# Optimization experiments

Measured on AMD Instinct MI355X. Metric: run time of the kernel, lower is better.

## Reference

```python
import jax, jax.numpy as jnp
import numpy as np

D_MODEL = 1024
NUM_HEADS = 16
D_K = D_MODEL // NUM_HEADS


def setup_inputs() -> dict:
    key = jax.random.key(0)
    ks = jax.random.split(key, 9)
    s = 1.0 / np.sqrt(D_MODEL)
    x = jax.random.normal(ks[0], (4, 2048, D_MODEL), dtype=jnp.float32)
    Wq = jax.random.uniform(ks[1], (D_MODEL, D_MODEL), jnp.float32, -s, s)
    bq = jax.random.uniform(ks[2], (D_MODEL,), jnp.float32, -s, s)
    Wk = jax.random.uniform(ks[3], (D_MODEL, D_MODEL), jnp.float32, -s, s)
    bk = jax.random.uniform(ks[4], (D_MODEL,), jnp.float32, -s, s)
    Wv = jax.random.uniform(ks[5], (D_MODEL, D_MODEL), jnp.float32, -s, s)
    bv = jax.random.uniform(ks[6], (D_MODEL,), jnp.float32, -s, s)
    Wo = jax.random.uniform(ks[7], (D_MODEL, D_MODEL), jnp.float32, -s, s)
    bo = jax.random.uniform(ks[8], (D_MODEL,), jnp.float32, -s, s)
    return {"x": x, "Wq": Wq, "bq": bq, "Wk": Wk, "bk": bk,
            "Wv": Wv, "bv": bv, "Wo": Wo, "bo": bo}


def reference(x, Wq, bq, Wk, bk, Wv, bv, Wo, bo):
    B, T, C = x.shape
    H, Dk = NUM_HEADS, D_K
    # linear projections (torch Linear: x @ W.T + b; here W stored as [in,out])
    q = (x @ Wq + bq).reshape(B, T, H, Dk).transpose(0, 2, 1, 3)  # [B,H,T,Dk]
    k = (x @ Wk + bk).reshape(B, T, H, Dk).transpose(0, 2, 1, 3)
    v = (x @ Wv + bv).reshape(B, T, H, Dk).transpose(0, 2, 1, 3)
    scores = jnp.einsum("bhtd,bhsd->bhts", q, k) / jnp.sqrt(jnp.float32(Dk))
    attn = jax.nn.softmax(scores, axis=-1)  # [B,H,T,T]
    context = jnp.einsum("bhts,bhsd->bhtd", attn, v)
    context = context.transpose(0, 2, 1, 3).reshape(B, T, C)
    return context @ Wo + bo
```

## Files before the change

kernel.cpp:

```cpp
#include <hip/hip_runtime.h>
#include <hip/hip_bf16.h>
#include <stdint.h>

typedef short bf16x8 __attribute__((ext_vector_type(8)));
typedef short bf16x4 __attribute__((ext_vector_type(4)));
typedef float f32x4  __attribute__((ext_vector_type(4)));

#define MFMA16(a, b, c) __builtin_amdgcn_mfma_f32_16x16x32_bf16((a), (b), (c), 0, 0, 0)

__device__ __forceinline__ unsigned short f2bf(float f) {
    union { float f; unsigned int u; } v; v.f = f;
    unsigned int u = v.u;
    u += 0x7fffu + ((u >> 16) & 1u);
    return (unsigned short)(u >> 16);
}

__device__ __forceinline__ unsigned int trunc_pk(float a, float b) {
    return (__float_as_uint(a) >> 16) | (__float_as_uint(b) & 0xffff0000u);
}

__device__ __forceinline__ float exp2f_fast(float x) {
#if __has_builtin(__builtin_amdgcn_exp2f)
    return __builtin_amdgcn_exp2f(x);
#else
    return exp2f(x);
#endif
}

__device__ __forceinline__ void g2lds16(const void* g, void* l) {
    __builtin_amdgcn_global_load_lds(
        (const __attribute__((address_space(1))) void*)g,
        (__attribute__((address_space(3))) void*)l, 16, 0, 0);
}


__global__ __launch_bounds__(256) void convert_x_kernel(
    const float4* __restrict__ src, ushort4* __restrict__ dst)
{
    int i = blockIdx.x * 256 + threadIdx.x;
    float4 v = src[i];
    ushort4 o;
    o.x = f2bf(v.x); o.y = f2bf(v.y); o.z = f2bf(v.z); o.w = f2bf(v.w);
    dst[i] = o;
}

__global__ __launch_bounds__(256) void transpose_w4_kernel(
    const float* __restrict__ W0, const float* __restrict__ W1,
    const float* __restrict__ W2, const float* __restrict__ W3,
    unsigned short* __restrict__ dst_base)
{
    __shared__ float tile[64][65];
    const int z = blockIdx.z;
    const float* src = (z == 0) ? W0 : (z == 1) ? W1 : (z == 2) ? W2 : W3;
    unsigned short* dst = dst_base + ((size_t)z << 20);
    const int k0 = blockIdx.x * 64, n0 = blockIdx.y * 64;
    const int tx = threadIdx.x & 63, ty = threadIdx.x >> 6;
    #pragma unroll
    for (int i = 0; i < 64; i += 4)
        tile[ty + i][tx] = src[(size_t)(k0 + ty + i) * 1024 + n0 + tx];
    __syncthreads();
    #pragma unroll
    for (int i = 0; i < 64; i += 4)
        dst[(size_t)(n0 + ty + i) * 1024 + k0 + tx] = f2bf(tile[tx][ty + i]);
}


#define QSCALE 0.18033688011112042f

template <int MODE>
__global__ __launch_bounds__(512, 2) void gemm256(
    const unsigned short* __restrict__ A, const unsigned short* __restrict__ Bt,
    const float* __restrict__ b0, const float* __restrict__ b1, const float* __restrict__ b2,
    unsigned short* __restrict__ Qb, unsigned short* __restrict__ Kb,
    unsigned short* __restrict__ Vt, float* __restrict__ out)
{
    __shared__ alignas(16) unsigned short As[2][256 * 64];
    __shared__ alignas(16) unsigned short Bs[2][128 * 64];

    const int t = threadIdx.x;
    const int m0 = blockIdx.y * 256, n0 = blockIdx.x * 128;
    const int lane = t & 63, w = t >> 6, quad = lane >> 4, c16 = lane & 15;
    const int moff = (w >> 1) * 64;
    const int noff = (w & 1) * 64;

    f32x4 acc[4][4];
    #pragma unroll
    for (int i = 0; i < 4; ++i)
        #pragma unroll
        for (int j = 0; j < 4; ++j)
            acc[i][j] = (f32x4){0.f, 0.f, 0.f, 0.f};

    const int sg = (t & 7) ^ ((t >> 3) & 7);
    const unsigned short* Agl = A  + (size_t)(m0 + (t >> 3)) * 1024 + sg * 8;
    const unsigned short* Bgl = Bt + (size_t)(n0 + (t >> 3)) * 1024 + sg * 8;
    unsigned short* Asl = &As[0][0] + t * 8;
    unsigned short* Bsl = &Bs[0][0] + t * 8;

    #pragma unroll
    for (int q = 0; q < 4; ++q)
        g2lds16(Agl + (size_t)q * 65536, Asl + q * 4096);
    #pragma unroll
    for (int q = 0; q < 2; ++q)
        g2lds16(Bgl + (size_t)q * 65536, Bsl + q * 4096);
    asm volatile("s_waitcnt vmcnt(0)" ::: "memory");
    __builtin_amdgcn_sched_barrier(0);
    __builtin_amdgcn_s_barrier();
    __builtin_amdgcn_sched_barrier(0);

    const int swz = c16 & 7;

    for (int kt = 0; kt < 16; ++kt) {
        const int buf = kt & 1;
        const unsigned short* Ab = &As[buf][0];
        const unsigned short* Bb = &Bs[buf][0];
        unsigned short* An = Asl + (buf ^ 1) * 16384;
        unsigned short* Bn = Bsl + (buf ^ 1) * 8192;
        const size_t knext = (size_t)(kt + 1) * 64;

        #pragma unroll
        for (int kh = 0; kh < 2; ++kh) {
            const int fgr = ((kh * 4 + quad) ^ swz) << 3;
            bf16x8 af[4], bfr[4];
            #pragma unroll
            for (int ms = 0; ms < 4; ++ms)
                af[ms] = *(const bf16x8*)(Ab + (moff + ms * 16 + c16) * 64 + fgr);
            #pragma unroll
            for (int ns = 0; ns < 4; ++ns)
                bfr[ns] = *(const bf16x8*)(Bb + (noff + ns * 16 + c16) * 64 + fgr);

            if (kt < 15) {
                if (kh == 0) {
                    g2lds16(Agl + knext,                      An);
                    g2lds16(Agl + knext + 65536,              An + 4096);
                    g2lds16(Bgl + knext,                      Bn);
                } else {
                    g2lds16(Agl + knext + 2 * 65536,          An + 2 * 4096);
                    g2lds16(Agl + knext + 3 * 65536,          An + 3 * 4096);
                    g2lds16(Bgl + knext + 65536,              Bn + 4096);
                }
            }

            __builtin_amdgcn_sched_barrier(0);
            __builtin_amdgcn_s_barrier();
            asm volatile("s_waitcnt lgkmcnt(0)" ::: "memory");
            __builtin_amdgcn_sched_barrier(0);

            __builtin_amdgcn_s_setprio(1);
            #pragma unroll
            for (int ms = 0; ms < 4; ++ms)
                #pragma unroll
                for (int ns = 0; ns < 4; ++ns)
                    acc[ms][ns] = MFMA16(af[ms], bfr[ns], acc[ms][ns]);
            __builtin_amdgcn_s_setprio(0);

            if (kh == 1) {
                asm volatile("s_waitcnt vmcnt(0)" ::: "memory");
            }
            __builtin_amdgcn_sched_barrier(0);
            __builtin_amdgcn_s_barrier();
            __builtin_amdgcn_sched_barrier(0);
        }
    }

    #pragma unroll
    for (int ns = 0; ns < 4; ++ns) {
        const int n = n0 + noff + ns * 16 + c16;
        if (MODE == 0) {
            const int mat = n >> 10, nn = n & 1023;
            const int h = nn >> 6, d = nn & 63;
            const float bias = (mat == 0) ? b0[nn] : ((mat == 1) ? b1[nn] : b2[nn]);
            #pragma unroll
            for (int ms = 0; ms < 4; ++ms) {
                const int mbase = m0 + moff + ms * 16 + quad * 4;
                const int b = mbase >> 11, tbase = mbase & 2047;
                const int bh = b * 16 + h;
                if (mat == 2) {
                    ushort4 pk;
                    pk.x = f2bf(acc[ms][ns][0] + bias);
                    pk.y = f2bf(acc[ms][ns][1] + bias);
                    pk.z = f2bf(acc[ms][ns][2] + bias);
                    pk.w = f2bf(acc[ms][ns][3] + bias);
                    *(ushort4*)(Vt + ((size_t)bh * 64 + d) * 2048 + tbase) = pk;
                } else {
                    #pragma unroll
                    for (int r = 0; r < 4; ++r) {
                        float v = acc[ms][ns][r] + bias;
                        if (mat == 0) v *= QSCALE;
                        unsigned short* dst = (mat == 0) ? Qb : Kb;
                        dst[((size_t)bh * 2048 + tbase + r) * 64 + d] = f2bf(v);
                    }
                }
            }
        } else {
            const float bias = b0[n];
            #pragma unroll
            for (int ms = 0; ms < 4; ++ms) {
                #pragma unroll
                for (int r = 0; r < 4; ++r) {
                    const int m = m0 + moff + ms * 16 + quad * 4 + r;
                    out[(size_t)m * 1024 + n] = acc[ms][ns][r] + bias;
                }
            }
        }
    }
}


__global__ __launch_bounds__(256, 4) void attn_kernel(
    const unsigned short* __restrict__ Qb, const unsigned short* __restrict__ Kb,
    const unsigned short* __restrict__ Vt, unsigned short* __restrict__ ctx)
{
    __shared__ alignas(16) unsigned short Ks[2][64 * 64];
    __shared__ alignas(16) unsigned short Vs[2][64 * 64];

    const int t = threadIdx.x, w = t >> 6, lane = t & 63;
    const int quad = lane >> 4, c16 = lane & 15;
    const int L = blockIdx.y * 16 + blockIdx.x;
    const int bh = ((L & 7) << 3) + (L >> 7);
    const int qt = (L >> 3) & 15;
    const int qbase = qt * 128 + w * 32;

    bf16x8 qf[2][2];
    #pragma unroll
    for (int mt = 0; mt < 2; ++mt) {
        const unsigned short* Qp = Qb + ((size_t)bh * 2048 + qbase + mt * 16 + c16) * 64;
        qf[mt][0] = *(const bf16x8*)(Qp + quad * 8);
        qf[mt][1] = *(const bf16x8*)(Qp + 32 + quad * 8);
    }

    float l_r[2] = {0.f, 0.f};
    f32x4 O[2][4];
    #pragma unroll
    for (int mt = 0; mt < 2; ++mt)
        #pragma unroll
        for (int dc = 0; dc < 4; ++dc) O[mt][dc] = (f32x4){0.f, 0.f, 0.f, 0.f};

    const int sgrp = (t & 7) ^ ((t >> 3) & 7);
    const unsigned short* Kgl = Kb + (size_t)bh * 131072 + (size_t)(t >> 3) * 64 + sgrp * 8;
    const unsigned short* Vgl = Vt + (size_t)bh * 131072 + (size_t)(t >> 3) * 2048 + sgrp * 8;
    const int tOff = t * 8;
    const f32x4 fzero = {0.f, 0.f, 0.f, 0.f};

    #pragma unroll
    for (int q = 0; q < 2; ++q) {
        g2lds16(Kgl + q * 2048,  Ks[0] + tOff + q * 2048);
        g2lds16(Vgl + (size_t)q * 65536, Vs[0] + tOff + q * 2048);
    }

    for (int it = 0; it < 32; ++it) {
        const int cur = it & 1;
        const unsigned short* Kc = Ks[cur];
        const unsigned short* Vc = Vs[cur];

        if (it < 31) {
            const int s0 = (it + 1) * 64;
            unsigned short* Kn = Ks[cur ^ 1] + tOff;
            unsigned short* Vn = Vs[cur ^ 1] + tOff;
            #pragma unroll
            for (int q = 0; q < 2; ++q) {
                g2lds16(Kgl + (size_t)s0 * 64 + q * 2048,    Kn + q * 2048);
                g2lds16(Vgl + s0 + (size_t)q * 65536,        Vn + q * 2048);
            }
            asm volatile("s_waitcnt vmcnt(4)" ::: "memory");
        } else {
            asm volatile("s_waitcnt vmcnt(0)" ::: "memory");
        }
        __builtin_amdgcn_sched_barrier(0);
        __builtin_amdgcn_s_barrier();
        __builtin_amdgcn_sched_barrier(0);

        #pragma unroll
        for (int ctp = 0; ctp < 2; ++ctp) {
            union { bf16x8 v; unsigned int d[4]; } af8[2];
            union { bf16x8 v; uint2 u[2]; } v8[4];

            #pragma unroll
            for (int ct2 = 0; ct2 < 2; ++ct2) {
                const int ct = ctp * 2 + ct2;
                const int key = ct * 16 + c16;
                const bf16x8 kf0 = *(const bf16x8*)(Kc + key * 64 + ((quad ^ (key & 7)) << 3));
                const bf16x8 kf1 = *(const bf16x8*)(Kc + key * 64 + (((4 + quad) ^ (key & 7)) << 3));

                const int g = ct * 2 + (quad >> 1);
                #pragma unroll
                for (int dc = 0; dc < 4; ++dc) {
                    const int d = dc * 16 + c16;
                    v8[dc].u[ct2] = *(const uint2*)(Vc + d * 64 + ((g ^ (d & 7)) << 3) + (quad & 1) * 4);
                }

                #pragma unroll
                for (int mt = 0; mt < 2; ++mt) {
                    f32x4 sa = MFMA16(kf0, qf[mt][0], fzero);
                    sa = MFMA16(kf1, qf[mt][1], sa);
                    const float p0 = exp2f_fast(sa[0]);
                    const float p1 = exp2f_fast(sa[1]);
                    const float p2 = exp2f_fast(sa[2]);
                    const float p3 = exp2f_fast(sa[3]);
                    l_r[mt] += (p0 + p1) + (p2 + p3);
                    af8[mt].d[ct2 * 2 + 0] = trunc_pk(p0, p1);
                    af8[mt].d[ct2 * 2 + 1] = trunc_pk(p2, p3);
                }
            }

            #pragma unroll
            for (int mt = 0; mt < 2; ++mt)
                #pragma unroll
                for (int dc = 0; dc < 4; ++dc)
                    O[mt][dc] = MFMA16(af8[mt].v, v8[dc].v, O[mt][dc]);
        }

        if (it < 31) {
            asm volatile("s_waitcnt lgkmcnt(0)" ::: "memory");
            __builtin_amdgcn_sched_barrier(0);
            __builtin_amdgcn_s_barrier();
            __builtin_amdgcn_sched_barrier(0);
        }
    }

    #pragma unroll
    for (int mt = 0; mt < 2; ++mt) {
        l_r[mt] += __shfl_xor(l_r[mt], 16);
        l_r[mt] += __shfl_xor(l_r[mt], 32);
    }

    const int b = bh >> 4, h = bh & 15;
    #pragma unroll
    for (int mt = 0; mt < 2; ++mt) {
        float inv[4];
        #pragma unroll
        for (int r = 0; r < 4; ++r)
            inv[r] = 1.0f / __shfl(l_r[mt], quad * 4 + r);
        #pragma unroll
        for (int dc = 0; dc < 4; ++dc)
            #pragma unroll
            for (int r = 0; r < 4; ++r) {
                const int row = qbase + mt * 16 + quad * 4 + r;
                ctx[((size_t)(b * 2048 + row)) * 1024 + h * 64 + dc * 16 + c16] =
                    f2bf(O[mt][dc][r] * inv[r]);
            }
    }
}


extern "C" void kernel_launch(void* const* d_in, const int* in_sizes, int n_in,
                              void* d_out, int out_size, void* d_ws, size_t ws_size,
                              hipStream_t stream)
{
    const float* x  = (const float*)d_in[0];
    const float* Wq = (const float*)d_in[1];
    const float* bq = (const float*)d_in[2];
    const float* Wk = (const float*)d_in[3];
    const float* bk = (const float*)d_in[4];
    const float* Wv = (const float*)d_in[5];
    const float* bv = (const float*)d_in[6];
    const float* Wo = (const float*)d_in[7];
    const float* bo = (const float*)d_in[8];
    float* out = (float*)d_out;

    char* ws = (char*)d_ws;
    unsigned short* xb    = (unsigned short*)(ws);
    unsigned short* Wqkvt = (unsigned short*)(ws + (16u << 20));
    unsigned short* Vt    = (unsigned short*)(ws + (24u << 20));
    unsigned short* Wot   = Wqkvt + (3u << 20);
    unsigned short* Qb    = (unsigned short*)((char*)d_out);
    unsigned short* Kb    = (unsigned short*)((char*)d_out + (16u << 20));

    convert_x_kernel<<<8192, 256, 0, stream>>>((const float4*)x, (ushort4*)xb);
    transpose_w4_kernel<<<dim3(16, 16, 4), 256, 0, stream>>>(Wq, Wk, Wv, Wo, Wqkvt);

    gemm256<0><<<dim3(24, 32), 512, 0, stream>>>(xb, Wqkvt, bq, bk, bv, Qb, Kb, Vt, nullptr);
    attn_kernel<<<dim3(16, 64), 256, 0, stream>>>(Qb, Kb, Vt, xb );
    gemm256<1><<<dim3(8, 32), 512, 0, stream>>>(xb, Wot, bo, nullptr, nullptr,
                                                nullptr, nullptr, nullptr, out);
}
```

Baseline: 277.0 us.

## Triple-buffer GEMM LDS prefetch and merge prep kernels into one launch

```diff
diff --git a/kernel.cpp b/kernel.cpp
--- a/kernel.cpp
+++ b/kernel.cpp
@@ -34,34 +34,35 @@
 }
 
 
-__global__ __launch_bounds__(256) void convert_x_kernel(
-    const float4* __restrict__ src, ushort4* __restrict__ dst)
-{
-    int i = blockIdx.x * 256 + threadIdx.x;
-    float4 v = src[i];
-    ushort4 o;
-    o.x = f2bf(v.x); o.y = f2bf(v.y); o.z = f2bf(v.z); o.w = f2bf(v.w);
-    dst[i] = o;
-}
-
-__global__ __launch_bounds__(256) void transpose_w4_kernel(
+__global__ __launch_bounds__(256) void prep_kernel(
+    const float4* __restrict__ src, ushort4* __restrict__ dst,
     const float* __restrict__ W0, const float* __restrict__ W1,
     const float* __restrict__ W2, const float* __restrict__ W3,
-    unsigned short* __restrict__ dst_base)
+    unsigned short* __restrict__ wdst_base)
 {
     __shared__ float tile[64][65];
-    const int z = blockIdx.z;
-    const float* src = (z == 0) ? W0 : (z == 1) ? W1 : (z == 2) ? W2 : W3;
-    unsigned short* dst = dst_base + ((size_t)z << 20);
-    const int k0 = blockIdx.x * 64, n0 = blockIdx.y * 64;
-    const int tx = threadIdx.x & 63, ty = threadIdx.x >> 6;
-    #pragma unroll
-    for (int i = 0; i < 64; i += 4)
-        tile[ty + i][tx] = src[(size_t)(k0 + ty + i) * 1024 + n0 + tx];
-    __syncthreads();
-    #pragma unroll
-    for (int i = 0; i < 64; i += 4)
-        dst[(size_t)(n0 + ty + i) * 1024 + k0 + tx] = f2bf(tile[tx][ty + i]);
+    const int id = blockIdx.x;
+    if (id < 8192) {
+        int i = id * 256 + threadIdx.x;
+        float4 v = src[i];
+        ushort4 o;
+        o.x = f2bf(v.x); o.y = f2bf(v.y); o.z = f2bf(v.z); o.w = f2bf(v.w);
+        dst[i] = o;
+    } else {
+        const int r = id - 8192;
+        const int z = r >> 8, rem = r & 255;
+        const float* wsrc = (z == 0) ? W0 : (z == 1) ? W1 : (z == 2) ? W2 : W3;
+        unsigned short* wdst = wdst_base + ((size_t)z << 20);
+        const int k0 = (rem & 15) * 64, n0 = (rem >> 4) * 64;
+        const int tx = threadIdx.x & 63, ty = threadIdx.x >> 6;
+        #pragma unroll
+        for (int i = 0; i < 64; i += 4)
+            tile[ty + i][tx] = wsrc[(size_t)(k0 + ty + i) * 1024 + n0 + tx];
+        __syncthreads();
+        #pragma unroll
+        for (int i = 0; i < 64; i += 4)
+            wdst[(size_t)(n0 + ty + i) * 1024 + k0 + tx] = f2bf(tile[tx][ty + i]);
+    }
 }
 
 
@@ -74,8 +75,8 @@
     unsigned short* __restrict__ Qb, unsigned short* __restrict__ Kb,
     unsigned short* __restrict__ Vt, float* __restrict__ out)
 {
-    __shared__ alignas(16) unsigned short As[2][256 * 64];
-    __shared__ alignas(16) unsigned short Bs[2][128 * 64];
+    __shared__ alignas(16) unsigned short As[3][256 * 64];
+    __shared__ alignas(16) unsigned short Bs[3][128 * 64];
 
     const int t = threadIdx.x;
     const int m0 = blockIdx.y * 256, n0 = blockIdx.x * 128;
@@ -93,29 +94,37 @@
     const int sg = (t & 7) ^ ((t >> 3) & 7);
     const unsigned short* Agl = A  + (size_t)(m0 + (t >> 3)) * 1024 + sg * 8;
     const unsigned short* Bgl = Bt + (size_t)(n0 + (t >> 3)) * 1024 + sg * 8;
-    unsigned short* Asl = &As[0][0] + t * 8;
-    unsigned short* Bsl = &Bs[0][0] + t * 8;
-
-    #pragma unroll
-    for (int q = 0; q < 4; ++q)
-        g2lds16(Agl + (size_t)q * 65536, Asl + q * 4096);
-    #pragma unroll
-    for (int q = 0; q < 2; ++q)
-        g2lds16(Bgl + (size_t)q * 65536, Bsl + q * 4096);
-    asm volatile("s_waitcnt vmcnt(0)" ::: "memory");
-    __builtin_amdgcn_sched_barrier(0);
-    __builtin_amdgcn_s_barrier();
-    __builtin_amdgcn_sched_barrier(0);
+    const int tOff = t * 8;
+
+    const unsigned short *pA0 = &As[0][0], *pA1 = &As[1][0], *pA2 = &As[2][0];
+    const unsigned short *pB0 = &Bs[0][0], *pB1 = &Bs[1][0], *pB2 = &Bs[2][0];
+
+#define STAGE(Ad, Bd, k0v)                                                  \
+    do {                                                                    \
+        unsigned short* Adp = (unsigned short*)(Ad) + tOff;                 \
+        unsigned short* Bdp = (unsigned short*)(Bd) + tOff;                 \
+        g2lds16(Agl + (k0v),              Adp);                             \
+        g2lds16(Agl + (k0v) + 65536,      Adp + 4096);                      \
+        g2lds16(Agl + (k0v) + 2 * 65536,  Adp + 2 * 4096);                  \
+        g2lds16(Agl + (k0v) + 3 * 65536,  Adp + 3 * 4096);                  \
+        g2lds16(Bgl + (k0v),              Bdp);                             \
+        g2lds16(Bgl + (k0v) + 65536,      Bdp + 4096);                      \
+    } while (0)
+
+    STAGE(pA0, pB0, 0);
+    STAGE(pA1, pB1, 64);
 
     const int swz = c16 & 7;
 
     for (int kt = 0; kt < 16; ++kt) {
-        const int buf = kt & 1;
-        const unsigned short* Ab = &As[buf][0];
-        const unsigned short* Bb = &Bs[buf][0];
-        unsigned short* An = Asl + (buf ^ 1) * 16384;
-        unsigned short* Bn = Bsl + (buf ^ 1) * 8192;
-        const size_t knext = (size_t)(kt + 1) * 64;
+        if (kt < 15) {
+            asm volatile("s_waitcnt vmcnt(6)" ::: "memory");
+        } else {
+            asm volatile("s_waitcnt vmcnt(0)" ::: "memory");
+        }
+        __builtin_amdgcn_sched_barrier(0);
+        __builtin_amdgcn_s_barrier();
+        __builtin_amdgcn_sched_barrier(0);
 
         #pragma unroll
         for (int kh = 0; kh < 2; ++kh) {
@@ -123,25 +132,14 @@
             bf16x8 af[4], bfr[4];
             #pragma unroll
             for (int ms = 0; ms < 4; ++ms)
-                af[ms] = *(const bf16x8*)(Ab + (moff + ms * 16 + c16) * 64 + fgr);
+                af[ms] = *(const bf16x8*)(pA0 + (moff + ms * 16 + c16) * 64 + fgr);
             #pragma unroll
             for (int ns = 0; ns < 4; ++ns)
-                bfr[ns] = *(const bf16x8*)(Bb + (noff + ns * 16 + c16) * 64 + fgr);
-
-            if (kt < 15) {
-                if (kh == 0) {
-                    g2lds16(Agl + knext,                      An);
-                    g2lds16(Agl + knext + 65536,              An + 4096);
-                    g2lds16(Bgl + knext,                      Bn);
-                } else {
-                    g2lds16(Agl + knext + 2 * 65536,          An + 2 * 4096);
-                    g2lds16(Agl + knext + 3 * 65536,          An + 3 * 4096);
-                    g2lds16(Bgl + knext + 65536,              Bn + 4096);
-                }
-            }
-
-            __builtin_amdgcn_sched_barrier(0);
-            __builtin_amdgcn_s_barrier();
+                bfr[ns] = *(const bf16x8*)(pB0 + (noff + ns * 16 + c16) * 64 + fgr);
+
+            if (kh == 0 && kt < 14)
+                STAGE(pA2, pB2, (size_t)(kt + 2) * 64);
+
             asm volatile("s_waitcnt lgkmcnt(0)" ::: "memory");
             __builtin_amdgcn_sched_barrier(0);
 
@@ -153,14 +151,17 @@
                     acc[ms][ns] = MFMA16(af[ms], bfr[ns], acc[ms][ns]);
             __builtin_amdgcn_s_setprio(0);
 
-            if (kh == 1) {
-                asm volatile("s_waitcnt vmcnt(0)" ::: "memory");
-            }
-            __builtin_amdgcn_sched_barrier(0);
-            __builtin_amdgcn_s_barrier();
-            __builtin_amdgcn_sched_barrier(0);
-        }
-    }
+            if (kh == 0) {
+                __builtin_amdgcn_sched_barrier(0);
+                __builtin_amdgcn_s_barrier();
+                __builtin_amdgcn_sched_barrier(0);
+            }
+        }
+
+        const unsigned short* ta = pA0; pA0 = pA1; pA1 = pA2; pA2 = ta;
+        const unsigned short* tb = pB0; pB0 = pB1; pB1 = pB2; pB2 = tb;
+    }
+#undef STAGE
 
     #pragma unroll
     for (int ns = 0; ns < 4; ++ns) {
@@ -365,8 +366,8 @@
     unsigned short* Qb    = (unsigned short*)((char*)d_out);
     unsigned short* Kb    = (unsigned short*)((char*)d_out + (16u << 20));
 
-    convert_x_kernel<<<8192, 256, 0, stream>>>((const float4*)x, (ushort4*)xb);
-    transpose_w4_kernel<<<dim3(16, 16, 4), 256, 0, stream>>>(Wq, Wk, Wv, Wo, Wqkvt);
+    prep_kernel<<<9216, 256, 0, stream>>>((const float4*)x, (ushort4*)xb,
+                                          Wq, Wk, Wv, Wo, Wqkvt);
 
     gemm256<0><<<dim3(24, 32), 512, 0, stream>>>(xb, Wqkvt, bq, bk, bv, Qb, Kb, Vt, nullptr);
     attn_kernel<<<dim3(16, 64), 256, 0, stream>>>(Qb, Kb, Vt, xb );
```

Result: faster. 271.2 us, median of 2 (-2.1%).
